# Kernel optimization log

Hardware: AMD Instinct MI355X
Metric: run time of the kernel (lower is better)

The kernel has to match this reference:

```python
import jax, jax.numpy as jnp
import numpy as np

N = 50000      # nodes in batched graph
E = 800000     # directed edges
F_IN = 64      # node_feature_dim
F_E = 16       # edge_feature_dim
H = 4          # heads
C = 64         # hidden_dim per head
HC = H * C     # 256


def setup_inputs() -> dict:
    key = jax.random.key(0)
    ks = jax.random.split(key, 26)
    rn = lambda k, s, scale=0.1: jax.random.normal(k, s, dtype=jnp.float32) * scale
    inp = {}
    inp["x"] = rn(ks[0], (N, F_IN), 1.0)
    inp["edge_src"] = jax.random.randint(ks[1], (E,), 0, N)
    inp["edge_dst"] = jax.random.randint(ks[2], (E,), 0, N)
    inp["edge_attr"] = rn(ks[3], (E, F_E), 1.0)
    # GATConv layer 1 params
    inp["W1"] = rn(ks[4], (F_IN, HC))
    inp["atts1"] = rn(ks[5], (H, C))
    inp["attd1"] = rn(ks[6], (H, C))
    inp["We1"] = rn(ks[7], (F_E, HC))
    inp["atte1"] = rn(ks[8], (H, C))
    inp["b1"] = jnp.zeros((HC,), jnp.float32)
    inp["g1"] = jnp.ones((HC,), jnp.float32)
    inp["be1"] = jnp.zeros((HC,), jnp.float32)
    # GATConv layer 2 params
    inp["W2"] = rn(ks[9], (HC, HC))
    inp["atts2"] = rn(ks[10], (H, C))
    inp["attd2"] = rn(ks[11], (H, C))
    inp["We2"] = rn(ks[12], (F_E, HC))
    inp["atte2"] = rn(ks[13], (H, C))
    inp["b2"] = jnp.zeros((HC,), jnp.float32)
    inp["g2"] = jnp.ones((HC,), jnp.float32)
    inp["be2"] = jnp.zeros((HC,), jnp.float32)
    # output head
    inp["Wout"] = rn(ks[14], (HC, 1))
    inp["bout"] = jnp.zeros((1,), jnp.float32)
    return inp


def _gat_layer(x, src, dst, eattr, W, att_s, att_d, We, att_e, b):
    """PyG GATConv (concat=True, add_self_loops with fill_value='mean', eval so no dropout)."""
    n = x.shape[0]
    e = src.shape[0]
    # self-loop edge attr = mean of incoming edge attrs per node (0 if none)
    deg = jax.ops.segment_sum(jnp.ones((e,), x.dtype), dst, num_segments=n)
    loop_attr = jax.ops.segment_sum(eattr, dst, num_segments=n) / jnp.maximum(deg, 1.0)[:, None]
    loop = jnp.arange(n)
    src2 = jnp.concatenate([src, loop])
    dst2 = jnp.concatenate([dst, loop])
    ea2 = jnp.concatenate([eattr, loop_attr], axis=0)
    xs = (x @ W).reshape(n, H, C)                          # [N,H,C]
    a_s = jnp.einsum('nhc,hc->nh', xs, att_s)              # [N,H]
    a_d = jnp.einsum('nhc,hc->nh', xs, att_d)
    ee = (ea2 @ We).reshape(-1, H, C)                      # [E+N,H,C]
    a_e = jnp.einsum('ehc,hc->eh', ee, att_e)
    logits = jax.nn.leaky_relu(a_s[src2] + a_d[dst2] + a_e, 0.2)  # [E+N,H]
    m = jax.ops.segment_max(logits, dst2, num_segments=n)
    p = jnp.exp(logits - m[dst2])
    denom = jax.ops.segment_sum(p, dst2, num_segments=n)[dst2] + 1e-16
    alpha = p / denom                                      # segment softmax per dst node
    out = jax.ops.segment_sum(xs[src2] * alpha[:, :, None], dst2, num_segments=n)
    return out.reshape(n, HC) + b


def _bn_relu(x, g, b):
    # BatchNorm1d in training mode (batch statistics), eps=1e-5
    mu = x.mean(axis=0)
    var = ((x - mu) ** 2).mean(axis=0)
    return jax.nn.relu(g * (x - mu) * jax.lax.rsqrt(var + 1e-5) + b)


def reference(x, edge_src, edge_dst, edge_attr,
              W1, atts1, attd1, We1, atte1, b1, g1, be1,
              W2, atts2, attd2, We2, atte2, b2, g2, be2,
              Wout, bout):
    h = _gat_layer(x, edge_src, edge_dst, edge_attr, W1, atts1, attd1, We1, atte1, b1)
    h = _bn_relu(h, g1, be1)
    h = _gat_layer(h, edge_src, edge_dst, edge_attr, W2, atts2, attd2, We2, atte2, b2)
    h = _bn_relu(h, g2, be2)
    return h @ Wout + bout
```

## Files before the change

### kernel.cpp

```cpp
#include <hip/hip_runtime.h>
#include <hip/hip_bf16.h>
#include <stdint.h>

#define NNODES 50000
#define NEDGES 800000
#define HC 256

typedef unsigned short u16;
typedef __attribute__((ext_vector_type(8))) short bf16x8;
typedef __attribute__((ext_vector_type(4))) float f32x4;
typedef __attribute__((ext_vector_type(4))) unsigned u32x4;

__device__ __forceinline__ float b2f(u16 v) {
    return __uint_as_float(((unsigned)v) << 16);
}
__device__ __forceinline__ u16 f2b(float f) {
    unsigned u = __float_as_uint(f);
    u += 0x7fff + ((u >> 16) & 1);
    return (u16)(u >> 16);
}
__device__ __forceinline__ float rdp(const void* p, long i, int bf) {
    return bf ? b2f(((const u16*)p)[i]) : ((const float*)p)[i];
}

__device__ __constant__ int dPO[19] = {0,16384,16640,16896,20992,21248,21504,21760,22016,
                                       87552,87808,88064,92160,92416,92672,92928,93184,93440,93441};
static const int hPO[19] = {0,16384,16640,16896,20992,21248,21504,21760,22016,
                            87552,87808,88064,92160,92416,92672,92928,93184,93440,93441};
#define TOTP 93441

__global__ __launch_bounds__(256) void prep0(unsigned* __restrict__ zp, long nwords,
                                             const unsigned* __restrict__ xbits,
                                             int* __restrict__ flag) {
    if (blockIdx.x < 128) {
        long i = (long)blockIdx.x * 256 + threadIdx.x;
        long stride = 128L * 256;
        for (; i < nwords; i += stride) zp[i] = 0u;
    } else {
        __shared__ int cnt;
        if (threadIdx.x == 0) cnt = 0;
        __syncthreads();
        int sane = 0;
        for (int i = threadIdx.x; i < 1024; i += 256) {
            unsigned lo = xbits[i] & 0xffffu;
            int e = (int)((lo >> 7) & 0xff);
            if (e >= 117 && e <= 133) sane++;
        }
        atomicAdd(&cnt, sane);
        __syncthreads();
        if (threadIdx.x == 0) *flag = (cnt >= 512) ? 1 : 0;
    }
}

struct Ptrs18 { const void* s[18]; };

#define NB_XB 512
#define NB_WT1 64
#define NB_WT2 256
#define NB_PALL ((TOTP + 255) / 256)
#define NB_DEG ((NEDGES + 255) / 256)
#define JB1 (NB_XB)
#define JB2 (JB1 + NB_WT1)
#define JB3 (JB2 + NB_WT2)
#define JB4 (JB3 + NB_PALL)
#define JB5 (JB4 + 1)
#define JB6 (JB5 + 1)
#define JB7 (JB6 + 4)
#define NB_PREP (JB7 + NB_DEG)

__global__ __launch_bounds__(256) void param_prep(
    Ptrs18 pp, const void* __restrict__ x_raw, const int* __restrict__ edst,
    const int* __restrict__ flag,
    u16* __restrict__ xb, u16* __restrict__ pall,
    u16* __restrict__ WT1, u16* __restrict__ WT2,
    float* __restrict__ ve1, float* __restrict__ ve2,
    float* __restrict__ us1, float* __restrict__ ud1,
    float* __restrict__ us2, float* __restrict__ ud2,
    int* __restrict__ deg) {
    int b = blockIdx.x, t = threadIdx.x;
    if (b >= JB7) {
        int e = (b - JB7) * 256 + t;
        if (e < NEDGES) atomicAdd(&deg[edst[e]], 1);
        return;
    }
    int bf = *flag;
    if (b < JB1) {
        long no = (long)NNODES * 64 / 8;
        long i = (long)b * 256 + t;
        long stride = (long)NB_XB * 256;
        if (bf) {
            const uint4* s = (const uint4*)x_raw;
            uint4* d = (uint4*)xb;
            for (; i < no; i += stride) d[i] = s[i];
        } else {
            const float4* s = (const float4*)x_raw;
            uint4* d = (uint4*)xb;
            for (; i < no; i += stride) {
                float4 a = s[i * 2], c = s[i * 2 + 1];
                uint4 o;
                o.x = (unsigned)f2b(a.x) | ((unsigned)f2b(a.y) << 16);
                o.y = (unsigned)f2b(a.z) | ((unsigned)f2b(a.w) << 16);
                o.z = (unsigned)f2b(c.x) | ((unsigned)f2b(c.y) << 16);
                o.w = (unsigned)f2b(c.z) | ((unsigned)f2b(c.w) << 16);
                d[i] = o;
            }
        }
        return;
    }
    if (b < JB2) {
        int i = (b - JB1) * 256 + t;
        int k = i >> 8, c = i & 255;
        WT1[c * 64 + k] = bf ? ((const u16*)pp.s[0])[i] : f2b(((const float*)pp.s[0])[i]);
        return;
    }
    if (b < JB3) {
        int i = (b - JB2) * 256 + t;
        int k = i >> 8, c = i & 255;
        WT2[c * 256 + k] = bf ? ((const u16*)pp.s[8])[i] : f2b(((const float*)pp.s[8])[i]);
        return;
    }
    if (b < JB4) {
        int i = (b - JB3) * 256 + t;
        if (i >= TOTP) return;
        int idx = 0;
        #pragma unroll
        for (int j = 1; j < 18; j++) idx += (i >= dPO[j]) ? 1 : 0;
        int rel = i - dPO[idx];
        pall[i] = bf ? ((const u16*)pp.s[idx])[rel] : f2b(((const float*)pp.s[idx])[rel]);
        return;
    }
    if (b < JB5) {
        if (t < 128) {
            int i = t & 63;
            int f = i >> 2, h = i & 3;
            const void* W = (t < 64) ? pp.s[3] : pp.s[11];
            const void* A = (t < 64) ? pp.s[4] : pp.s[12];
            float* o = (t < 64) ? ve1 : ve2;
            float s = 0.f;
            for (int c = 0; c < 64; c++)
                s += rdp(W, f * 256 + h * 64 + c, bf) * rdp(A, h * 64 + c, bf);
            o[i] = s;
        }
        return;
    }
    if (b < JB6) {
        int f = t >> 2, h = t & 3;
        float sa = 0.f, sb = 0.f;
        for (int c = 0; c < 64; c++) {
            float w = rdp(pp.s[0], f * 256 + h * 64 + c, bf);
            sa += w * rdp(pp.s[1], h * 64 + c, bf);
            sb += w * rdp(pp.s[2], h * 64 + c, bf);
        }
        us1[t] = sa;
        ud1[t] = sb;
        return;
    }
    {
        int i = (b - JB6) * 256 + t;
        if (i >= 1024) return;
        int f = i >> 2, h = i & 3;
        float sa = 0.f, sb = 0.f;
        for (int c = 0; c < 64; c++) {
            float w = rdp(pp.s[8], f * 256 + h * 64 + c, bf);
            sa += w * rdp(pp.s[9], h * 64 + c, bf);
            sb += w * rdp(pp.s[10], h * 64 + c, bf);
        }
        us2[i] = sa;
        ud2[i] = sb;
    }
}

__global__ void block_sum(const int* __restrict__ deg, int* __restrict__ bsums, int n) {
    __shared__ int lds[256];
    int i = blockIdx.x * 256 + threadIdx.x;
    lds[threadIdx.x] = (i < n) ? deg[i] : 0;
    __syncthreads();
    for (int s = 128; s; s >>= 1) {
        if (threadIdx.x < s) lds[threadIdx.x] += lds[threadIdx.x + s];
        __syncthreads();
    }
    if (threadIdx.x == 0) bsums[blockIdx.x] = lds[0];
}

__global__ void scan_write(const int* __restrict__ bsums, const int* __restrict__ deg,
                           int* __restrict__ off, int* __restrict__ cursor, int n, int nb) {
    __shared__ int sb[256];
    __shared__ int lds[256];
    int t = threadIdx.x;
    int v = (t < nb) ? bsums[t] : 0;
    sb[t] = v;
    __syncthreads();
    for (int s = 1; s < 256; s <<= 1) {
        int u = (t >= s) ? sb[t - s] : 0;
        __syncthreads();
        sb[t] += u;
        __syncthreads();
    }
    int boff = sb[blockIdx.x] - bsums[blockIdx.x];
    int i = blockIdx.x * 256 + t;
    int dv = (i < n) ? deg[i] : 0;
    lds[t] = dv;
    __syncthreads();
    for (int s = 1; s < 256; s <<= 1) {
        int u = (t >= s) ? lds[t - s] : 0;
        __syncthreads();
        lds[t] += u;
        __syncthreads();
    }
    int exc = lds[t] - dv + boff;
    if (i < n) { off[i] = exc; cursor[i] = exc; }
}

__global__ __launch_bounds__(256) void edge_stage(
    const void* __restrict__ eattr_raw, const int* __restrict__ flag,
    const int* __restrict__ esrc, const int* __restrict__ edst,
    const float* __restrict__ ve1, const float* __restrict__ ve2,
    int* __restrict__ cursor, uint4* __restrict__ rec) {
    int e = blockIdx.x * 256 + threadIdx.x;
    if (e >= NEDGES) return;
    float a[16];
    if (*flag) {
        const u16* s = (const u16*)eattr_raw + (long)e * 16;
        const uint4* q = (const uint4*)s;
        uint4 q0 = q[0], q1 = q[1];
        unsigned w0[8] = {q0.x, q0.y, q0.z, q0.w, q1.x, q1.y, q1.z, q1.w};
        #pragma unroll
        for (int j = 0; j < 8; j++) {
            a[2 * j] = b2f((u16)(w0[j] & 0xffff));
            a[2 * j + 1] = b2f((u16)(w0[j] >> 16));
        }
    } else {
        const float* s = (const float*)eattr_raw + (long)e * 16;
        #pragma unroll
        for (int j = 0; j < 16; j += 4) {
            float4 q = *(const float4*)(s + j);
            a[j] = q.x; a[j + 1] = q.y; a[j + 2] = q.z; a[j + 3] = q.w;
        }
    }
    float s1[4], s2[4];
    #pragma unroll
    for (int h = 0; h < 4; h++) {
        float t1 = 0.f, t2 = 0.f;
        #pragma unroll
        for (int f = 0; f < 16; f++) {
            t1 += a[f] * ve1[f * 4 + h];
            t2 += a[f] * ve2[f * 4 + h];
        }
        s1[h] = t1;
        s2[h] = t2;
    }
    unsigned a1lo = (unsigned)f2b(s1[0]) | ((unsigned)f2b(s1[1]) << 16);
    unsigned a1hi = (unsigned)f2b(s1[2]) | ((unsigned)f2b(s1[3]) << 16);
    unsigned a2lo = (unsigned)f2b(s2[0]) | ((unsigned)f2b(s2[1]) << 16);
    unsigned a2hi = (unsigned)f2b(s2[2]) | ((unsigned)f2b(s2[3]) << 16);
    int d = edst[e];
    int p = atomicAdd(&cursor[d], 1);
    unsigned src = (unsigned)esrc[e];
    u32x4 r0 = {src, a1lo, a1hi, 0u};
    u32x4 r1 = {src, a2lo, a2hi, 0u};
    __builtin_nontemporal_store(r0, (u32x4*)(rec + (long)p * 2));
    __builtin_nontemporal_store(r1, (u32x4*)(rec + (long)p * 2 + 1));
}

__device__ __forceinline__ void gload_lds16(const u16* g, u16* l) {
    __builtin_amdgcn_global_load_lds(
        (const __attribute__((address_space(1))) unsigned*)g,
        (__attribute__((address_space(3))) unsigned*)l, 16, 0, 0);
}

template <int K, bool BN>
__global__ __launch_bounds__(256) void gemm_tile(const u16* __restrict__ A,
                                                 const u16* __restrict__ WT,
                                                 const float* __restrict__ coef,
                                                 u16* __restrict__ out) {
    __shared__ u16 As[128 * 32];
    __shared__ u16 Bs[128 * 32];
    int tid = threadIdx.x;
    int wave = tid >> 6, lane = tid & 63;
    int wr = wave >> 1, wc = wave & 1;
    int quad = lane >> 4, l15 = lane & 15;
    long row0 = (long)(blockIdx.x >> 1) * 128;
    int col0 = (blockIdx.x & 1) * 128;
    int srow = lane >> 2;
    int soct = (lane & 3) * 8;
    f32x4 acc[4][4] = {};
    for (int kk = 0; kk < K; kk += 32) {
        #pragma unroll
        for (int sub = 0; sub < 2; sub++) {
            int rr = wave * 32 + sub * 16;
            long gr = row0 + rr + srow;
            if (gr >= NNODES) gr = NNODES - 1;
            gload_lds16(A + gr * K + kk + soct, &As[rr * 32]);
            gload_lds16(WT + (long)(col0 + rr + srow) * K + kk + soct, &Bs[rr * 32]);
        }
        __syncthreads();
        bf16x8 av[4], bv[4];
        #pragma unroll
        for (int m = 0; m < 4; m++)
            av[m] = *(const bf16x8*)&As[(wr * 64 + m * 16 + l15) * 32 + quad * 8];
        if (BN) {
            int kb = kk + quad * 8;
            float4 sc0 = *(const float4*)(coef + kb);
            float4 sc1 = *(const float4*)(coef + kb + 4);
            float4 sh0 = *(const float4*)(coef + 256 + kb);
            float4 sh1 = *(const float4*)(coef + 256 + kb + 4);
            float scl[8] = {sc0.x, sc0.y, sc0.z, sc0.w, sc1.x, sc1.y, sc1.z, sc1.w};
            float shf[8] = {sh0.x, sh0.y, sh0.z, sh0.w, sh1.x, sh1.y, sh1.z, sh1.w};
            #pragma unroll
            for (int m = 0; m < 4; m++) {
                #pragma unroll
                for (int j = 0; j < 8; j++) {
                    float v = b2f((u16)av[m][j]);
                    v = fmaxf(v * scl[j] + shf[j], 0.f);
                    av[m][j] = (short)f2b(v);
                }
            }
        }
        #pragma unroll
        for (int n = 0; n < 4; n++)
            bv[n] = *(const bf16x8*)&Bs[(wc * 64 + n * 16 + l15) * 32 + quad * 8];
        #pragma unroll
        for (int m = 0; m < 4; m++)
            #pragma unroll
            for (int n = 0; n < 4; n++)
                acc[m][n] = __builtin_amdgcn_mfma_f32_16x16x32_bf16(av[m], bv[n],
                                                                    acc[m][n], 0, 0, 0);
        __syncthreads();
    }
    #pragma unroll
    for (int m = 0; m < 4; m++) {
        #pragma unroll
        for (int j = 0; j < 4; j++) {
            long r = row0 + wr * 64 + m * 16 + quad * 4 + j;
            if (r < NNODES) {
                u16* op = out + r * HC + col0 + wc * 64 + l15;
                #pragma unroll
                for (int n = 0; n < 4; n++) op[n * 16] = f2b(acc[m][n][j]);
            }
        }
    }
}

template <int K, bool BN>
__global__ __launch_bounds__(256) void proj_att(const u16* __restrict__ X,
                                                const float* __restrict__ coef,
                                                const float* __restrict__ us,
                                                const float* __restrict__ ud,
                                                float* __restrict__ as_, float* __restrict__ ad_) {
    int gw = (blockIdx.x * 256 + threadIdx.x) >> 6;
    int lane = threadIdx.x & 63;
    int node, f0;
    if (K == 64) {
        node = gw * 4 + (lane >> 4);
        f0 = (lane & 15) * 4;
    } else {
        node = gw;
        f0 = lane * 4;
    }
    if (node >= NNODES) return;
    uint2 v = *(const uint2*)(X + (long)node * K + f0);
    float xv[4] = {b2f((u16)(v.x & 0xffffu)), b2f((u16)(v.x >> 16)),
                   b2f((u16)(v.y & 0xffffu)), b2f((u16)(v.y >> 16))};
    float pas[4] = {0.f, 0.f, 0.f, 0.f}, pad[4] = {0.f, 0.f, 0.f, 0.f};
    #pragma unroll
    for (int j = 0; j < 4; j++) {
        int f = f0 + j;
        float x = xv[j];
        if (BN) x = fmaxf(x * coef[f] + coef[256 + f], 0.f);
        #pragma unroll
        for (int h = 0; h < 4; h++) {
            pas[h] += x * us[f * 4 + h];
            pad[h] += x * ud[f * 4 + h];
        }
    }
    const int omax = (K == 64) ? 8 : 32;
    #pragma unroll
    for (int h = 0; h < 4; h++) {
        for (int o = omax; o; o >>= 1) {
            pas[h] += __shfl_xor(pas[h], o);
            pad[h] += __shfl_xor(pad[h], o);
        }
    }
    bool wr = (K == 64) ? ((lane & 15) == 0) : (lane == 0);
    if (wr) {
        #pragma unroll
        for (int h = 0; h < 4; h++) {
            as_[node * 4 + h] = pas[h];
            ad_[node * 4 + h] = pad[h];
        }
    }
}

__global__ __launch_bounds__(256) void gat_fused(
    const u16* __restrict__ xs, const float* __restrict__ as_, const float* __restrict__ ad_,
    const uint4* __restrict__ rec, int layer,
    const int* __restrict__ off, const int* __restrict__ deg,
    const u16* __restrict__ bias, u16* __restrict__ out) {
    __shared__ int s_lds[4][64];
    __shared__ float w_lds[4][64][4];
    int wid = (blockIdx.x * 256 + threadIdx.x) >> 6;
    if (wid >= NNODES) return;
    int wave = threadIdx.x >> 6;
    int lane = threadIdx.x & 63;
    int d = wid;
    int st = off[d], dg = deg[d];
    int slot = lane >> 2, h = lane & 3;
    float adv = ad_[d * 4 + h];
    float m = -1e30f, s = 0.f, sae = 0.f;
    const uint4* rbase = rec + (long)st * 2 + layer;

    if (dg <= 64) {
        for (int i = slot; i < dg; i += 16) {
            uint4 r4 = rbase[(long)i * 2];
            int src = (int)r4.x;
            unsigned wsel = (h & 2) ? r4.z : r4.y;
            float aev = b2f((u16)((h & 1) ? (wsel >> 16) : (wsel & 0xffffu)));
            float t = as_[src * 4 + h] + adv + aev;
            float lg = (t > 0.f) ? t : 0.2f * t;
            if (h == 0) s_lds[wave][i] = src;
            w_lds[wave][i][h] = lg;
            sae += aev;
            float mn = fmaxf(m, lg);
            s = s * __expf(m - mn) + __expf(lg - mn);
            m = mn;
        }
        #pragma unroll
        for (int o = 4; o < 64; o <<= 1) {
            float mo = __shfl_xor(m, o), so = __shfl_xor(s, o), ao = __shfl_xor(sae, o);
            float mn = fmaxf(m, mo);
            s = s * __expf(m - mn) + so * __expf(mo - mn);
            m = mn;
            sae += ao;
        }
        float invs, wself;
        {
            float asv = as_[d * 4 + h];
            float l0 = asv + adv + sae / fmaxf((float)dg, 1.f);
            l0 = (l0 > 0.f) ? l0 : 0.2f * l0;
            float mn = fmaxf(m, l0);
            s = s * __expf(m - mn) + __expf(l0 - mn);
            m = mn;
            invs = 1.f / s;
            wself = __expf(l0 - mn) * invs;
        }
        for (int i = slot; i < dg; i += 16)
            w_lds[wave][i][h] = __expf(w_lds[wave][i][h] - m) * invs;

        int cg = lane & 31, half = lane >> 5;
        int ch8 = cg * 8;
        int h2 = cg >> 3;
        float ws2 = __shfl(wself, h2);
        const u16* xbase = xs + ch8;
        float a0, a1, a2, a3, a4, a5, a6, a7;
        {
            uint4 v = *(const uint4*)(xbase + (long)d * HC);
            float wsf = half ? 0.f : ws2;
            a0 = wsf * b2f((u16)(v.x & 0xffffu)); a1 = wsf * b2f((u16)(v.x >> 16));
            a2 = wsf * b2f((u16)(v.y & 0xffffu)); a3 = wsf * b2f((u16)(v.y >> 16));
            a4 = wsf * b2f((u16)(v.z & 0xffffu)); a5 = wsf * b2f((u16)(v.z >> 16));
            a6 = wsf * b2f((u16)(v.w & 0xffffu)); a7 = wsf * b2f((u16)(v.w >> 16));
        }
        int i = half;
        for (; i + 6 < dg; i += 8) {
            float wA = w_lds[wave][i][h2];     int sA = s_lds[wave][i];
            float wB = w_lds[wave][i + 2][h2]; int sB = s_lds[wave][i + 2];
            float wC = w_lds[wave][i + 4][h2]; int sC = s_lds[wave][i + 4];
            float wD = w_lds[wave][i + 6][h2]; int sD = s_lds[wave][i + 6];
            uint4 vA = *(const uint4*)(xbase + (long)sA * HC);
            uint4 vB = *(const uint4*)(xbase + (long)sB * HC);
            uint4 vC = *(const uint4*)(xbase + (long)sC * HC);
            uint4 vD = *(const uint4*)(xbase + (long)sD * HC);
            a0 += wA * b2f((u16)(vA.x & 0xffffu)) + wB * b2f((u16)(vB.x & 0xffffu))
                + wC * b2f((u16)(vC.x & 0xffffu)) + wD * b2f((u16)(vD.x & 0xffffu));
            a1 += wA * b2f((u16)(vA.x >> 16))     + wB * b2f((u16)(vB.x >> 16))
                + wC * b2f((u16)(vC.x >> 16))     + wD * b2f((u16)(vD.x >> 16));
            a2 += wA * b2f((u16)(vA.y & 0xffffu)) + wB * b2f((u16)(vB.y & 0xffffu))
                + wC * b2f((u16)(vC.y & 0xffffu)) + wD * b2f((u16)(vD.y & 0xffffu));
            a3 += wA * b2f((u16)(vA.y >> 16))     + wB * b2f((u16)(vB.y >> 16))
                + wC * b2f((u16)(vC.y >> 16))     + wD * b2f((u16)(vD.y >> 16));
            a4 += wA * b2f((u16)(vA.z & 0xffffu)) + wB * b2f((u16)(vB.z & 0xffffu))
                + wC * b2f((u16)(vC.z & 0xffffu)) + wD * b2f((u16)(vD.z & 0xffffu));
            a5 += wA * b2f((u16)(vA.z >> 16))     + wB * b2f((u16)(vB.z >> 16))
                + wC * b2f((u16)(vC.z >> 16))     + wD * b2f((u16)(vD.z >> 16));
            a6 += wA * b2f((u16)(vA.w & 0xffffu)) + wB * b2f((u16)(vB.w & 0xffffu))
                + wC * b2f((u16)(vC.w & 0xffffu)) + wD * b2f((u16)(vD.w & 0xffffu));
            a7 += wA * b2f((u16)(vA.w >> 16))     + wB * b2f((u16)(vB.w >> 16))
                + wC * b2f((u16)(vC.w >> 16))     + wD * b2f((u16)(vD.w >> 16));
        }
        for (; i < dg; i += 2) {
            float wA = w_lds[wave][i][h2]; int sA = s_lds[wave][i];
            uint4 vA = *(const uint4*)(xbase + (long)sA * HC);
            a0 += wA * b2f((u16)(vA.x & 0xffffu)); a1 += wA * b2f((u16)(vA.x >> 16));
            a2 += wA * b2f((u16)(vA.y & 0xffffu)); a3 += wA * b2f((u16)(vA.y >> 16));
            a4 += wA * b2f((u16)(vA.z & 0xffffu)); a5 += wA * b2f((u16)(vA.z >> 16));
            a6 += wA * b2f((u16)(vA.w & 0xffffu)); a7 += wA * b2f((u16)(vA.w >> 16));
        }
        a0 += __shfl_xor(a0, 32); a1 += __shfl_xor(a1, 32);
        a2 += __shfl_xor(a2, 32); a3 += __shfl_xor(a3, 32);
        a4 += __shfl_xor(a4, 32); a5 += __shfl_xor(a5, 32);
        a6 += __shfl_xor(a6, 32); a7 += __shfl_xor(a7, 32);
        if (half == 0) {
            uint4 bv = *(const uint4*)(bias + ch8);
            a0 += b2f((u16)(bv.x & 0xffffu)); a1 += b2f((u16)(bv.x >> 16));
            a2 += b2f((u16)(bv.y & 0xffffu)); a3 += b2f((u16)(bv.y >> 16));
            a4 += b2f((u16)(bv.z & 0xffffu)); a5 += b2f((u16)(bv.z >> 16));
            a6 += b2f((u16)(bv.w & 0xffffu)); a7 += b2f((u16)(bv.w >> 16));
            uint4 ov;
            ov.x = (unsigned)f2b(a0) | ((unsigned)f2b(a1) << 16);
            ov.y = (unsigned)f2b(a2) | ((unsigned)f2b(a3) << 16);
            ov.z = (unsigned)f2b(a4) | ((unsigned)f2b(a5) << 16);
            ov.w = (unsigned)f2b(a6) | ((unsigned)f2b(a7) << 16);
            *(uint4*)(out + (long)d * HC + ch8) = ov;
        }
        return;
    }

    for (int base = 0; base < dg; base += 16) {
        int i = base + slot;
        float lg = -1e30f, aev = 0.f, w = 0.f;
        if (i < dg) {
            uint4 r4 = rbase[(long)i * 2];
            int src = (int)r4.x;
            unsigned wsel = (h & 2) ? r4.z : r4.y;
            aev = b2f((u16)((h & 1) ? (wsel >> 16) : (wsel & 0xffffu)));
            float t = as_[src * 4 + h] + adv + aev;
            lg = (t > 0.f) ? t : 0.2f * t;
        }
        sae += aev;
        float mn = fmaxf(m, lg);
        if (i < dg) w = __expf(lg - mn);
        s = s * __expf(m - mn) + w;
        m = mn;
    }
    #pragma unroll
    for (int o = 4; o < 64; o <<= 1) {
        float mo = __shfl_xor(m, o), so = __shfl_xor(s, o), ao = __shfl_xor(sae, o);
        float mn = fmaxf(m, mo);
        s = s * __expf(m - mn) + so * __expf(mo - mn);
        m = mn;
        sae += ao;
    }
    float invs, wself;
    {
        float asv = as_[d * 4 + h];
        float l0 = asv + adv + sae / fmaxf((float)dg, 1.f);
        l0 = (l0 > 0.f) ? l0 : 0.2f * l0;
        float mn = fmaxf(m, l0);
        s = s * __expf(m - mn) + __expf(l0 - mn);
        m = mn;
        invs = 1.f / s;
        wself = __expf(l0 - mn) * invs;
    }
    int h2 = lane >> 4;
    float m2 = __shfl(m, h2);
    float is2 = __shfl(invs, h2);
    float ws2 = __shfl(wself, h2);
    float adv2 = __shfl(adv, h2);
    int cb = lane * 4;
    float a0, a1, a2, a3;
    {
        uint2 v = *(const uint2*)(xs + (long)d * HC + cb);
        a0 = ws2 * b2f((u16)(v.x & 0xffffu)); a1 = ws2 * b2f((u16)(v.x >> 16));
        a2 = ws2 * b2f((u16)(v.y & 0xffffu)); a3 = ws2 * b2f((u16)(v.y >> 16));
    }
    int slot16 = lane & 15;
    int lhi = lane & 48;
    for (int base = 0; base < dg; base += 16) {
        int cnt = min(16, dg - base);
        float wv = 0.f;
        int srcl = 0;
        if (slot16 < cnt) {
            uint4 r4 = rbase[(long)(base + slot16) * 2];
            srcl = (int)r4.x;
            unsigned wsel = (h2 & 2) ? r4.z : r4.y;
            float aev = b2f((u16)((h2 & 1) ? (wsel >> 16) : (wsel & 0xffffu)));
            float t = as_[srcl * 4 + h2] + adv2 + aev;
            t = (t > 0.f) ? t : 0.2f * t;
            wv = __expf(t - m2) * is2;
        }
        for (int j = 0; j < cnt; j++) {
            float w0 = __shfl(wv, lhi | j);
            int s0 = __shfl(srcl, j);
            uint2 v0 = *(const uint2*)(xs + (long)s0 * HC + cb);
            a0 += w0 * b2f((u16)(v0.x & 0xffffu));
            a1 += w0 * b2f((u16)(v0.x >> 16));
            a2 += w0 * b2f((u16)(v0.y & 0xffffu));
            a3 += w0 * b2f((u16)(v0.y >> 16));
        }
    }
    u16 o0 = f2b(a0 + b2f(bias[cb + 0]));
    u16 o1 = f2b(a1 + b2f(bias[cb + 1]));
    u16 o2 = f2b(a2 + b2f(bias[cb + 2]));
    u16 o3 = f2b(a3 + b2f(bias[cb + 3]));
    uint2 ov;
    ov.x = (unsigned)o0 | ((unsigned)o1 << 16);
    ov.y = (unsigned)o2 | ((unsigned)o3 << 16);
    *(uint2*)(out + (long)d * HC + cb) = ov;
}

__global__ __launch_bounds__(256) void bn_stats(const u16* __restrict__ h,
                                                float* __restrict__ stats,
                                                int* __restrict__ cnt,
                                                const u16* __restrict__ g,
                                                const u16* __restrict__ be,
                                                float* __restrict__ coef) {
    __shared__ float lsum[256], lsq[256];
    __shared__ int last;
    int t = threadIdx.x;
    int p = t & 127;
    int ro = t >> 7;
    float s0 = 0.f, q0 = 0.f, s1 = 0.f, q1 = 0.f;
    const u16* hp = h + 2 * p;
    for (long r = (long)blockIdx.x * 8 + ro * 4; r < NNODES; r += (long)gridDim.x * 8) {
        unsigned v0 = *(const unsigned*)(hp + (r + 0) * HC);
        unsigned v1 = *(const unsigned*)(hp + (r + 1) * HC);
        unsigned v2 = *(const unsigned*)(hp + (r + 2) * HC);
        unsigned v3 = *(const unsigned*)(hp + (r + 3) * HC);
        float l0 = b2f((u16)(v0 & 0xffffu)), h0 = b2f((u16)(v0 >> 16));
        float l1 = b2f((u16)(v1 & 0xffffu)), h1 = b2f((u16)(v1 >> 16));
        float l2 = b2f((u16)(v2 & 0xffffu)), h2 = b2f((u16)(v2 >> 16));
        float l3 = b2f((u16)(v3 & 0xffffu)), h3 = b2f((u16)(v3 >> 16));
        s0 += l0 + l1 + l2 + l3;
        q0 += l0 * l0 + l1 * l1 + l2 * l2 + l3 * l3;
        s1 += h0 + h1 + h2 + h3;
        q1 += h0 * h0 + h1 * h1 + h2 * h2 + h3 * h3;
    }
    if (ro == 1) {
        lsum[2 * p] = s0; lsum[2 * p + 1] = s1;
        lsq[2 * p] = q0;  lsq[2 * p + 1] = q1;
    }
    __syncthreads();
    if (ro == 0) {
        atomicAdd(&stats[2 * p],           s0 + lsum[2 * p]);
        atomicAdd(&stats[2 * p + 1],       s1 + lsum[2 * p + 1]);
        atomicAdd(&stats[256 + 2 * p],     q0 + lsq[2 * p]);
        atomicAdd(&stats[256 + 2 * p + 1], q1 + lsq[2 * p + 1]);
    }
    __threadfence();
    __syncthreads();
    if (t == 0) {
        int old = atomicAdd(cnt, 1);
        last = (old == (int)gridDim.x - 1);
    }
    __syncthreads();
    if (last) {
        float sum = atomicAdd(&stats[t], 0.f);
        float sq  = atomicAdd(&stats[256 + t], 0.f);
        float mu = sum * (1.0f / NNODES);
        float var = sq * (1.0f / NNODES) - mu * mu;
        var = fmaxf(var, 0.f);
        float rs = rsqrtf(var + 1e-5f);
        float sc = b2f(g[t]) * rs;
        coef[t] = sc;
        coef[256 + t] = b2f(be[t]) - sc * mu;
    }
}

__global__ __launch_bounds__(256) void out_head(const u16* __restrict__ h,
                                                const float* __restrict__ coef,
                                                const u16* __restrict__ wout,
                                                const u16* __restrict__ bout,
                                                void* __restrict__ y,
                                                const int* __restrict__ flag) {
    int wid = (blockIdx.x * 256 + threadIdx.x) >> 6;
    int lane = threadIdx.x & 63;
    if (wid >= NNODES) return;
    int c0 = lane * 4;
    uint2 v = *(const uint2*)(h + (long)wid * HC + c0);
    uint2 wv = *(const uint2*)(wout + c0);
    float hv[4] = {b2f((u16)(v.x & 0xffffu)), b2f((u16)(v.x >> 16)),
                   b2f((u16)(v.y & 0xffffu)), b2f((u16)(v.y >> 16))};
    float wf[4] = {b2f((u16)(wv.x & 0xffffu)), b2f((u16)(wv.x >> 16)),
                   b2f((u16)(wv.y & 0xffffu)), b2f((u16)(wv.y >> 16))};
    float p = 0.f;
    #pragma unroll
    for (int j = 0; j < 4; j++) {
        float t = fmaxf(hv[j] * coef[c0 + j] + coef[256 + c0 + j], 0.f);
        p += t * wf[j];
    }
    for (int o = 32; o; o >>= 1) p += __shfl_down(p, o);
    if (lane == 0) {
        float t = p + b2f(bout[0]);
        if (*flag) ((u16*)y)[wid] = f2b(t);
        else       ((float*)y)[wid] = t;
    }
}

extern "C" void kernel_launch(void* const* d_in, const int* in_sizes, int n_in,
                              void* d_out, int out_size, void* d_ws, size_t ws_size,
                              hipStream_t stream) {
    (void)in_sizes; (void)n_in; (void)out_size; (void)ws_size;
    const void* x_raw     = d_in[0];
    const int*  esrc      = (const int*)d_in[1];
    const int*  edst      = (const int*)d_in[2];
    const void* eattr_raw = d_in[3];

    char* ws = (char*)d_ws;
    size_t o = 0;
    auto alloc = [&](size_t bytes) -> char* {
        o = (o + 255) & ~(size_t)255;
        char* p = ws + o;
        o += bytes;
        return p;
    };
    int* dflag = (int*)alloc(256);
    u16* xb   = (u16*)alloc((size_t)NNODES * 64 * 2);
    u16* pall = (u16*)alloc((size_t)TOTP * 2);
    u16 *b1b = pall + hPO[5], *g1b = pall + hPO[6], *be1b = pall + hPO[7],
        *b2b = pall + hPO[13], *g2b = pall + hPO[14], *be2b = pall + hPO[15],
        *Woutb = pall + hPO[16], *boutb = pall + hPO[17];
    u16* WT1 = (u16*)alloc(256 * 64 * 2);
    u16* WT2 = (u16*)alloc(256 * 256 * 2);
    float* ve1 = (float*)alloc(64 * 4);
    float* ve2 = (float*)alloc(64 * 4);
    float* us1 = (float*)alloc(256 * 4);
    float* ud1 = (float*)alloc(256 * 4);
    float* us2 = (float*)alloc(1024 * 4);
    float* ud2 = (float*)alloc(1024 * 4);
    float* coef1 = (float*)alloc(512 * 4);
    float* coef2 = (float*)alloc(512 * 4);
    int* deg = (int*)alloc((size_t)NNODES * 4);
    float* stats1 = (float*)alloc(512 * 4);
    float* stats2 = (float*)alloc(512 * 4);
    int* bnc1 = (int*)alloc(256);
    int* bnc2 = (int*)alloc(256);
    size_t zero_end = o;
    size_t zero_begin = (size_t)((char*)deg - ws);
    int* off = (int*)alloc((size_t)NNODES * 4);
    int* cursor = (int*)alloc((size_t)NNODES * 4);
    int* bsums = (int*)alloc(256 * 4);
    uint4* rec = (uint4*)alloc((size_t)NEDGES * 32);
    float* as_ = (float*)alloc((size_t)NNODES * 16);
    float* ad_ = (float*)alloc((size_t)NNODES * 16);
    u16* bufA = (u16*)alloc((size_t)NNODES * HC * 2);
    u16* bufB = (u16*)alloc((size_t)NNODES * HC * 2);

    long zwords = (long)((zero_end - zero_begin) / 4);
    prep0<<<129, 256, 0, stream>>>((unsigned*)(ws + zero_begin), zwords,
                                   (const unsigned*)x_raw, dflag);

    Ptrs18 pp;
    for (int i = 0; i < 18; i++) pp.s[i] = d_in[4 + i];
    param_prep<<<NB_PREP, 256, 0, stream>>>(pp, x_raw, edst, dflag, xb, pall, WT1, WT2,
                                            ve1, ve2, us1, ud1, us2, ud2, deg);

    int eblocks = (NEDGES + 255) / 256;
    int nb = (NNODES + 255) / 256;
    block_sum<<<nb, 256, 0, stream>>>(deg, bsums, NNODES);
    scan_write<<<nb, 256, 0, stream>>>(bsums, deg, off, cursor, NNODES, nb);
    edge_stage<<<eblocks, 256, 0, stream>>>(eattr_raw, dflag, esrc, edst, ve1, ve2,
                                            cursor, rec);

    int gtiles = ((NNODES + 127) / 128) * 2;
    int wblocks = (NNODES * 64 + 255) / 256;
    int pblocks64 = (NNODES + 15) / 16;

    gemm_tile<64, false><<<gtiles, 256, 0, stream>>>(xb, WT1, nullptr, bufA);
    proj_att<64, false><<<pblocks64, 256, 0, stream>>>(xb, nullptr, us1, ud1, as_, ad_);
    gat_fused<<<wblocks, 256, 0, stream>>>(bufA, as_, ad_, rec, 0, off, deg, b1b, bufB);
    bn_stats<<<512, 256, 0, stream>>>(bufB, stats1, bnc1, g1b, be1b, coef1);

    gemm_tile<256, true><<<gtiles, 256, 0, stream>>>(bufB, WT2, coef1, bufA);
    proj_att<256, true><<<wblocks, 256, 0, stream>>>(bufB, coef1, us2, ud2, as_, ad_);
    gat_fused<<<wblocks, 256, 0, stream>>>(bufA, as_, ad_, rec, 1, off, deg, b2b, bufB);
    bn_stats<<<512, 256, 0, stream>>>(bufB, stats2, bnc2, g2b, be2b, coef2);

    out_head<<<wblocks, 256, 0, stream>>>(bufB, coef2, Woutb, boutb, d_out, dflag);
}
```

Baseline: 553.1 us.

## Merge independent edge, GEMM and projection kernels into block-dispatched launches

Turns edge_stage, gemm_tile and proj_att into device bodies and dispatches them by block index inside two combined kernels, one per layer, so independent work shares a launch and its blocks can run concurrently. This removes launch gaps and the tail underutilisation of each small kernel. It also swaps the nontemporal stores of edge records for ordinary stores, which may change cache behaviour. The combined kernels carry the union of the LDS and register needs of their parts, which could lower occupancy for the lighter edge and projection blocks.

```diff
diff --git a/kernel.cpp b/kernel.cpp
--- a/kernel.cpp
+++ b/kernel.cpp
@@ -9,7 +9,6 @@
 typedef unsigned short u16;
 typedef __attribute__((ext_vector_type(8))) short bf16x8;
 typedef __attribute__((ext_vector_type(4))) float f32x4;
-typedef __attribute__((ext_vector_type(4))) unsigned u32x4;
 
 __device__ __forceinline__ float b2f(u16 v) {
     return __uint_as_float(((unsigned)v) << 16);
@@ -211,12 +210,12 @@
     if (i < n) { off[i] = exc; cursor[i] = exc; }
 }
 
-__global__ __launch_bounds__(256) void edge_stage(
+__device__ __forceinline__ void edge_body(
     const void* __restrict__ eattr_raw, const int* __restrict__ flag,
     const int* __restrict__ esrc, const int* __restrict__ edst,
     const float* __restrict__ ve1, const float* __restrict__ ve2,
-    int* __restrict__ cursor, uint4* __restrict__ rec) {
-    int e = blockIdx.x * 256 + threadIdx.x;
+    int* __restrict__ cursor, uint4* __restrict__ rec, int eb) {
+    int e = eb * 256 + threadIdx.x;
     if (e >= NEDGES) return;
     float a[16];
     if (*flag) {
@@ -256,10 +255,8 @@
     int d = edst[e];
     int p = atomicAdd(&cursor[d], 1);
     unsigned src = (unsigned)esrc[e];
-    u32x4 r0 = {src, a1lo, a1hi, 0u};
-    u32x4 r1 = {src, a2lo, a2hi, 0u};
-    __builtin_nontemporal_store(r0, (u32x4*)(rec + (long)p * 2));
-    __builtin_nontemporal_store(r1, (u32x4*)(rec + (long)p * 2 + 1));
+    rec[(long)p * 2 + 0] = make_uint4(src, a1lo, a1hi, 0u);
+    rec[(long)p * 2 + 1] = make_uint4(src, a2lo, a2hi, 0u);
 }
 
 __device__ __forceinline__ void gload_lds16(const u16* g, u16* l) {
@@ -269,18 +266,18 @@
 }
 
 template <int K, bool BN>
-__global__ __launch_bounds__(256) void gemm_tile(const u16* __restrict__ A,
-                                                 const u16* __restrict__ WT,
-                                                 const float* __restrict__ coef,
-                                                 u16* __restrict__ out) {
+__device__ __forceinline__ void gemm_body(const u16* __restrict__ A,
+                                          const u16* __restrict__ WT,
+                                          const float* __restrict__ coef,
+                                          u16* __restrict__ out, int bid) {
     __shared__ u16 As[128 * 32];
     __shared__ u16 Bs[128 * 32];
     int tid = threadIdx.x;
     int wave = tid >> 6, lane = tid & 63;
     int wr = wave >> 1, wc = wave & 1;
     int quad = lane >> 4, l15 = lane & 15;
-    long row0 = (long)(blockIdx.x >> 1) * 128;
-    int col0 = (blockIdx.x & 1) * 128;
+    long row0 = (long)(bid >> 1) * 128;
+    int col0 = (bid & 1) * 128;
     int srow = lane >> 2;
     int soct = (lane & 3) * 8;
     f32x4 acc[4][4] = {};
@@ -342,12 +339,13 @@
 }
 
 template <int K, bool BN>
-__global__ __launch_bounds__(256) void proj_att(const u16* __restrict__ X,
-                                                const float* __restrict__ coef,
-                                                const float* __restrict__ us,
-                                                const float* __restrict__ ud,
-                                                float* __restrict__ as_, float* __restrict__ ad_) {
-    int gw = (blockIdx.x * 256 + threadIdx.x) >> 6;
+__device__ __forceinline__ void proj_body(const u16* __restrict__ X,
+                                          const float* __restrict__ coef,
+                                          const float* __restrict__ us,
+                                          const float* __restrict__ ud,
+                                          float* __restrict__ as_, float* __restrict__ ad_,
+                                          int pb) {
+    int gw = (pb * 256 + (int)threadIdx.x) >> 6;
     int lane = threadIdx.x & 63;
     int node, f0;
     if (K == 64) {
@@ -389,6 +387,46 @@
             ad_[node * 4 + h] = pad[h];
         }
     }
+}
+
+#define GT 782
+#define EB 3125
+#define PB64 3125
+
+__global__ __launch_bounds__(256) void l1_mix(
+    const void* __restrict__ eattr_raw, const int* __restrict__ flag,
+    const int* __restrict__ esrc, const int* __restrict__ edst,
+    const float* __restrict__ ve1, const float* __restrict__ ve2,
+    int* __restrict__ cursor, uint4* __restrict__ rec,
+    const u16* __restrict__ xb, const u16* __restrict__ WT1, u16* __restrict__ bufA,
+    const float* __restrict__ us1, const float* __restrict__ ud1,
+    float* __restrict__ as_, float* __restrict__ ad_) {
+    int b = blockIdx.x;
+    if (b < EB) {
+        edge_body(eattr_raw, flag, esrc, edst, ve1, ve2, cursor, rec, b);
+        return;
+    }
+    b -= EB;
+    if (b < GT) {
+        gemm_body<64, false>(xb, WT1, nullptr, bufA, b);
+        return;
+    }
+    b -= GT;
+    proj_body<64, false>(xb, nullptr, us1, ud1, as_, ad_, b);
+}
+
+__global__ __launch_bounds__(256) void l2_mix(
+    const u16* __restrict__ h1, const u16* __restrict__ WT2,
+    const float* __restrict__ coef, u16* __restrict__ bufA,
+    const float* __restrict__ us2, const float* __restrict__ ud2,
+    float* __restrict__ as_, float* __restrict__ ad_) {
+    int b = blockIdx.x;
+    if (b < GT) {
+        gemm_body<256, true>(h1, WT2, coef, bufA, b);
+        return;
+    }
+    b -= GT;
+    proj_body<256, true>(h1, coef, us2, ud2, as_, ad_, b);
 }
 
 __global__ __launch_bounds__(256) void gat_fused(
@@ -744,24 +782,19 @@
     param_prep<<<NB_PREP, 256, 0, stream>>>(pp, x_raw, edst, dflag, xb, pall, WT1, WT2,
                                             ve1, ve2, us1, ud1, us2, ud2, deg);
 
-    int eblocks = (NEDGES + 255) / 256;
     int nb = (NNODES + 255) / 256;
     block_sum<<<nb, 256, 0, stream>>>(deg, bsums, NNODES);
     scan_write<<<nb, 256, 0, stream>>>(bsums, deg, off, cursor, NNODES, nb);
-    edge_stage<<<eblocks, 256, 0, stream>>>(eattr_raw, dflag, esrc, edst, ve1, ve2,
-                                            cursor, rec);
-
-    int gtiles = ((NNODES + 127) / 128) * 2;
+
     int wblocks = (NNODES * 64 + 255) / 256;
-    int pblocks64 = (NNODES + 15) / 16;
-
-    gemm_tile<64, false><<<gtiles, 256, 0, stream>>>(xb, WT1, nullptr, bufA);
-    proj_att<64, false><<<pblocks64, 256, 0, stream>>>(xb, nullptr, us1, ud1, as_, ad_);
+
+    l1_mix<<<EB + GT + PB64, 256, 0, stream>>>(eattr_raw, dflag, esrc, edst, ve1, ve2,
+                                               cursor, rec, xb, WT1, bufA,
+                                               us1, ud1, as_, ad_);
     gat_fused<<<wblocks, 256, 0, stream>>>(bufA, as_, ad_, rec, 0, off, deg, b1b, bufB);
     bn_stats<<<512, 256, 0, stream>>>(bufB, stats1, bnc1, g1b, be1b, coef1);
 
-    gemm_tile<256, true><<<gtiles, 256, 0, stream>>>(bufB, WT2, coef1, bufA);
-    proj_att<256, true><<<wblocks, 256, 0, stream>>>(bufB, coef1, us2, ud2, as_, ad_);
+    l2_mix<<<GT + wblocks, 256, 0, stream>>>(bufB, WT2, coef1, bufA, us2, ud2, as_, ad_);
     gat_fused<<<wblocks, 256, 0, stream>>>(bufA, as_, ad_, rec, 1, off, deg, b2b, bufB);
     bn_stats<<<512, 256, 0, stream>>>(bufB, stats2, bnc2, g2b, be2b, coef2);
 
```

Result: faster. 530.7 us, median of 2 (-4.0%).
